# Kernel tuning notes

Measured on AMD Instinct MI355X. Metric: run time of the kernel, lower is better.

## Reference

```python
import jax, jax.numpy as jnp
import numpy as np

N, E = 50000, 1600000
IN, HID, HEADS, OUT = 128, 32, 4, 32
NEG_SLOPE = 0.2  # PyG GATConv default leaky_relu slope


def _glorot(k, shape):
    fan = shape[0] + shape[-1]
    return jax.random.normal(k, shape, dtype=jnp.float32) * np.sqrt(2.0 / fan).astype(np.float32)


def setup_inputs() -> dict:
    key = jax.random.key(0)
    ks = jax.random.split(key, 16)
    x = jax.random.normal(ks[0], (N, IN), dtype=jnp.float32)
    edge_index = jax.random.randint(ks[1], (2, E), 0, N, dtype=jnp.int32)
    # layer 0: in -> heads*hid, concat
    W0 = _glorot(ks[2], (IN, HEADS * HID))
    as0 = _glorot(ks[3], (HEADS, HID)); ad0 = _glorot(ks[4], (HEADS, HID))
    b0 = jnp.zeros((HEADS * HID,), jnp.float32)
    # layer 1: heads*hid -> heads*hid, concat
    W1 = _glorot(ks[5], (HEADS * HID, HEADS * HID))
    as1 = _glorot(ks[6], (HEADS, HID)); ad1 = _glorot(ks[7], (HEADS, HID))
    b1 = jnp.zeros((HEADS * HID,), jnp.float32)
    # layer 2: heads*hid -> out, heads=1, concat=False
    W2 = _glorot(ks[8], (HEADS * HID, OUT))
    as2 = _glorot(ks[9], (1, OUT)); ad2 = _glorot(ks[10], (1, OUT))
    b2 = jnp.zeros((OUT,), jnp.float32)
    return dict(x=x, edge_index=edge_index, W0=W0, as0=as0, ad0=ad0, b0=b0,
                W1=W1, as1=as1, ad1=ad1, b1=b1, W2=W2, as2=as2, ad2=ad2, b2=b2)


def gat_layer(x, src, dst, W, a_src, a_dst, b, heads, out_ch, concat):
    # linear transform per head: [N, heads, out_ch]
    h = (x @ W).reshape(N, heads, out_ch)
    # per-node attention half-logits: [N, heads]
    alpha_src = jnp.einsum('nhc,hc->nh', h, a_src)
    alpha_dst = jnp.einsum('nhc,hc->nh', h, a_dst)
    # per-edge logits (edge j -> i): [E', heads]
    logits = jax.nn.leaky_relu(alpha_src[src] + alpha_dst[dst], NEG_SLOPE)
    # segment softmax over incoming edges of each destination node
    m = jax.ops.segment_max(logits, dst, num_segments=N)
    e = jnp.exp(logits - m[dst])
    denom = jax.ops.segment_sum(e, dst, num_segments=N)
    alpha = e / denom[dst]
    # weighted message scatter-add: [N, heads, out_ch]
    out = jax.ops.segment_sum(h[src] * alpha[:, :, None], dst, num_segments=N)
    out = out.reshape(N, heads * out_ch) if concat else out.mean(axis=1)
    return out + b, alpha


def reference(x, edge_index, W0, as0, ad0, b0, W1, as1, ad1, b1, W2, as2, ad2, b2):
    # add self loops (PyG add_self_loops=True)
    loops = jnp.arange(N, dtype=edge_index.dtype)
    src = jnp.concatenate([edge_index[0], loops])
    dst = jnp.concatenate([edge_index[1], loops])

    h, alpha0 = gat_layer(x, src, dst, W0, as0, ad0, b0, HEADS, HID, True)
    h = jax.nn.elu(h)  # dropout inactive in eval mode
    h, _ = gat_layer(h, src, dst, W1, as1, ad1, b1, HEADS, HID, True)
    h = jax.nn.elu(h)
    out, _ = gat_layer(h, src, dst, W2, as2, ad2, b2, 1, OUT, False)
    return alpha0, out
```

## Files before the change

kernel.cpp:

```cpp
#include <hip/hip_runtime.h>
#include <math.h>

#define NN 50000
#define NEG 0.2f
#define TILE 4096

typedef __attribute__((ext_vector_type(8))) short short8;
typedef __attribute__((ext_vector_type(4))) float f32x4;

__device__ __forceinline__ unsigned short f2bf(float f){
    unsigned u = __float_as_uint(f);
    u += 0x7fffu + ((u >> 16) & 1u);
    return (unsigned short)(u >> 16);
}
__device__ __forceinline__ float bf2f(unsigned short v){
    return __uint_as_float(((unsigned)v) << 16);
}

__device__ __forceinline__ int excl_scan_256(int v, int* buf, int tid){
    buf[tid] = v;
    __syncthreads();
#pragma unroll
    for (int off = 1; off < 256; off <<= 1){
        int t = (tid >= off) ? buf[tid - off] : 0;
        __syncthreads();
        buf[tid] += t;
        __syncthreads();
    }
    return buf[tid] - v;
}

__global__ __launch_bounds__(256) void k_binning(const int* __restrict__ ei, int E,
        int* __restrict__ bucketCount, unsigned* __restrict__ tmp){
    __shared__ unsigned stage[TILE];
    __shared__ int hist[256], sbuf[256], exs[256], cur[256], gbase[256];
    int tid = threadIdx.x;
    int EP = E + NN;
    int tileBase = blockIdx.x * TILE;
    int cnt = min(TILE, EP - tileBase);

    hist[tid] = 0;
    __syncthreads();

    unsigned packed[16];
#pragma unroll
    for (int k = 0; k < 16; ++k){
        int e = tileBase + tid + (k << 8);
        unsigned p = 0xffffffffu;
        if (e < EP){
            int s, d;
            if (e < E){ s = ei[e]; d = ei[E + e]; } else { s = e - E; d = s; }
            p = ((unsigned)d << 16) | (unsigned)s;
            atomicAdd(&hist[d >> 8], 1);
        }
        packed[k] = p;
    }
    __syncthreads();
    int h = hist[tid];
    int ex = excl_scan_256(h, sbuf, tid);
    exs[tid] = ex;
    cur[tid] = ex;
    __syncthreads();
#pragma unroll
    for (int k = 0; k < 16; ++k){
        unsigned p = packed[k];
        if (p != 0xffffffffu){
            int b = p >> 24;
            int pos = atomicAdd(&cur[b], 1);
            stage[pos] = p;
        }
    }
    gbase[tid] = atomicAdd(&bucketCount[tid], h);
    __syncthreads();
    for (int i = tid; i < cnt; i += 256){
        unsigned p = stage[i];
        int b = p >> 24;
        tmp[(b << 14) + gbase[b] + (i - exs[b])] = p;
    }
}

__global__ __launch_bounds__(256) void k_bucket_csr(int EP,
        const int* __restrict__ bucketCount, const unsigned* __restrict__ tmp,
        int* __restrict__ row_ptr, unsigned short* __restrict__ ssrc){
    __shared__ int sbuf[256], deg[256], cur[256];
    __shared__ int baseSh, nSh;
    int b = blockIdx.x;
    int tid = threadIdx.x;
    int c = bucketCount[tid];
    int exb = excl_scan_256(c, sbuf, tid);
    if (tid == b){ baseSh = exb; nSh = c; }
    deg[tid] = 0;
    __syncthreads();
    int base = baseSh, n = nSh;
    const unsigned* tb = tmp + ((size_t)b << 14);
    for (int i = tid; i < n; i += 256)
        atomicAdd(&deg[(tb[i] >> 16) & 255], 1);
    __syncthreads();
    int d = deg[tid];
    int dx = excl_scan_256(d, sbuf, tid);
    cur[tid] = dx;
    int dst = (b << 8) + tid;
    if (dst < NN) row_ptr[dst] = base + dx;
    if (b == 0 && tid == 0) row_ptr[NN] = EP;
    __syncthreads();
    for (int i = tid; i < n; i += 256){
        unsigned p = tb[i];
        int pos = atomicAdd(&cur[(p >> 16) & 255], 1);
        ssrc[base + pos] = (unsigned short)(p & 0xffffu);
    }
}

__global__ void k_packW(const float* __restrict__ W0, const float* __restrict__ W1,
                        const float* __restrict__ W2,
                        unsigned short* __restrict__ h0, unsigned short* __restrict__ l0,
                        unsigned short* __restrict__ h1, unsigned short* __restrict__ l1,
                        unsigned short* __restrict__ h2, unsigned short* __restrict__ l2){
    int t = blockIdx.x * 256 + threadIdx.x;
    const float* W; unsigned short *ph, *pl; int Ncol; int u;
    if (t < 16384){ W = W0; ph = h0; pl = l0; Ncol = 128; u = t; }
    else if (t < 32768){ W = W1; ph = h1; pl = l1; Ncol = 128; u = t - 16384; }
    else if (t < 36864){ W = W2; ph = h2; pl = l2; Ncol = 32;  u = t - 32768; }
    else return;
    int n = u >> 7, k = u & 127;
    float f = W[k * Ncol + n];
    unsigned short hi = f2bf(f);
    unsigned short lo = f2bf(f - bf2f(hi));
    ph[n * 128 + k] = hi;
    pl[n * 128 + k] = lo;
}

template<int NT, int HH>
__global__ __launch_bounds__(256) void k_gemm_mfma(
        const float* __restrict__ A,
        const unsigned short* __restrict__ Bhi,
        const unsigned short* __restrict__ Blo,
        float* __restrict__ C, unsigned short* __restrict__ Cbf,
        const float* __restrict__ a_s,
        const float* __restrict__ a_d,
        float* __restrict__ asrc, float* __restrict__ adst,
        float* __restrict__ asrc_i, float* __restrict__ adst_i, int M){
    const int Ncol = NT * 16;
    int wave = threadIdx.x >> 6;
    int lane = threadIdx.x & 63;
    int r    = lane & 15;
    int oct  = lane >> 4;
    int rowBase = blockIdx.x * 64 + wave * 16;

    f32x4 acc[NT];
#pragma unroll
    for (int c = 0; c < NT; ++c) acc[c] = (f32x4){0.f, 0.f, 0.f, 0.f};

    int lrow = rowBase + r; if (lrow > M - 1) lrow = M - 1;
    const float* arow = A + (size_t)lrow * 128;

    for (int t = 0; t < 4; ++t){
        int k0 = t * 32 + oct * 8;
        float4 a0 = *(const float4*)&arow[k0];
        float4 a1 = *(const float4*)&arow[k0 + 4];
        float av[8] = {a0.x, a0.y, a0.z, a0.w, a1.x, a1.y, a1.z, a1.w};
        short8 ahi, alo;
#pragma unroll
        for (int j = 0; j < 8; ++j){
            unsigned short h = f2bf(av[j]);
            unsigned short l = f2bf(av[j] - bf2f(h));
            ahi[j] = (short)h; alo[j] = (short)l;
        }
#pragma unroll
        for (int c = 0; c < NT; ++c){
            short8 bhi = *(const short8*)&Bhi[(c * 16 + r) * 128 + k0];
            short8 blo = *(const short8*)&Blo[(c * 16 + r) * 128 + k0];
            acc[c] = __builtin_amdgcn_mfma_f32_16x16x32_bf16(ahi, bhi, acc[c], 0, 0, 0);
            acc[c] = __builtin_amdgcn_mfma_f32_16x16x32_bf16(alo, bhi, acc[c], 0, 0, 0);
            acc[c] = __builtin_amdgcn_mfma_f32_16x16x32_bf16(ahi, blo, acc[c], 0, 0, 0);
        }
    }
#pragma unroll
    for (int c = 0; c < NT; ++c){
#pragma unroll
        for (int reg = 0; reg < 4; ++reg){
            int row = rowBase + oct * 4 + reg;
            if (row < M){
                int colg = c * 16 + r;
                float v = acc[c][reg];
                if (C)   C[(size_t)row * Ncol + colg] = v;
                if (Cbf) Cbf[(size_t)(colg >> 5) * ((size_t)M * 32)
                             + (size_t)row * 32 + (colg & 31)] = f2bf(v);
            }
        }
    }

    float as_v[NT], ad_v[NT];
#pragma unroll
    for (int c = 0; c < NT; ++c){
        as_v[c] = a_s[c * 16 + r];
        ad_v[c] = a_d[c * 16 + r];
    }
    float vs[HH * 4], vd[HH * 4];
#pragma unroll
    for (int h = 0; h < HH; ++h)
#pragma unroll
        for (int reg = 0; reg < 4; ++reg){
            vs[h * 4 + reg] = acc[2 * h][reg] * as_v[2 * h]
                            + acc[2 * h + 1][reg] * as_v[2 * h + 1];
            vd[h * 4 + reg] = acc[2 * h][reg] * ad_v[2 * h]
                            + acc[2 * h + 1][reg] * ad_v[2 * h + 1];
        }
#pragma unroll
    for (int off = 1; off < 16; off <<= 1){
#pragma unroll
        for (int k = 0; k < HH * 4; ++k){
            vs[k] += __shfl_xor(vs[k], off);
            vd[k] += __shfl_xor(vd[k], off);
        }
    }
    if (HH == 4){
        int reg = r & 3, hd = r >> 2;
        int row = rowBase + oct * 4 + reg;
        if (row < M){
            asrc[hd * M + row] = vs[hd * 4 + reg];
            adst[hd * M + row] = vd[hd * 4 + reg];
            if (asrc_i){
                asrc_i[row * 4 + hd] = vs[hd * 4 + reg];
                adst_i[row * 4 + hd] = vd[hd * 4 + reg];
            }
        }
    } else {
        int reg = r & 3;
        int row = rowBase + oct * 4 + reg;
        if (row < M){
            if (r < 4)       asrc[row] = vs[reg];
            else if (r < 8)  adst[row] = vd[reg];
        }
    }
}

__global__ __launch_bounds__(256) void k_aggh4(
        const uint4* __restrict__ hb4,
        const float* __restrict__ asrc,
        const float* __restrict__ adst,
        const int* __restrict__ row_ptr, const unsigned short* __restrict__ ssrc,
        const float* __restrict__ bias, float* __restrict__ outp,
        float* __restrict__ gdenom, int writeStats){
    int b  = blockIdx.x;
    int h  = (b >> 1) & 3;
    int kh = (b >> 3) * 2 + (b & 1);
    int wave = threadIdx.x >> 6;
    int lane = threadIdx.x & 63;
    int ns = lane >> 4;
    int g  = (lane >> 2) & 3;
    int q  = lane & 3;
    int i  = kh * 16 + wave * 4 + ns;
    bool valid = (i < NN);
    int iv = valid ? i : NN - 1;
    int lo = row_ptr[iv], hi = row_ptr[iv + 1];
    float adv = adst[h * NN + iv];
    const uint4* hp = hb4 + (size_t)h * ((size_t)NN * 4);
    const float* ap = asrc + h * NN;

    float acc[8];
#pragma unroll
    for (int k = 0; k < 8; ++k) acc[k] = 0.f;
    float dsum = 0.f;

#define AGH_FMA(AA, GV) {                                                     \
        acc[0] += (AA) * __uint_as_float((GV).x << 16);                       \
        acc[1] += (AA) * __uint_as_float((GV).x & 0xffff0000u);               \
        acc[2] += (AA) * __uint_as_float((GV).y << 16);                       \
        acc[3] += (AA) * __uint_as_float((GV).y & 0xffff0000u);               \
        acc[4] += (AA) * __uint_as_float((GV).z << 16);                       \
        acc[5] += (AA) * __uint_as_float((GV).z & 0xffff0000u);               \
        acc[6] += (AA) * __uint_as_float((GV).w << 16);                       \
        acc[7] += (AA) * __uint_as_float((GV).w & 0xffff0000u); }
#define AGH_ONE(JJ) {                                                         \
        float lg_ = ap[(JJ)] + adv;                                           \
        lg_ = fmaxf(lg_, NEG * lg_);                                          \
        float a_ = __expf(lg_);                                               \
        dsum += a_;                                                           \
        uint4 gv_ = hp[(JJ) * 4u + (unsigned)q];                              \
        AGH_FMA(a_, gv_) }

    int idx = lo;
    if (lo & 1){
        if (g == 0){ unsigned j = ssrc[lo]; AGH_ONE(j) }
        idx = lo + 1;
    }
    for (; idx + 16 <= hi; idx += 16){
        unsigned pA = *(const unsigned*)&ssrc[idx + 2 * g];
        unsigned pB = *(const unsigned*)&ssrc[idx + 8 + 2 * g];
        unsigned j0 = pA & 0xffffu, j1 = pA >> 16;
        unsigned j2 = pB & 0xffffu, j3 = pB >> 16;
        float s0 = ap[j0], s1 = ap[j1], s2 = ap[j2], s3 = ap[j3];
        uint4 v0 = hp[j0 * 4u + (unsigned)q];
        uint4 v1 = hp[j1 * 4u + (unsigned)q];
        uint4 v2 = hp[j2 * 4u + (unsigned)q];
        uint4 v3 = hp[j3 * 4u + (unsigned)q];
        float lg0 = s0 + adv; lg0 = fmaxf(lg0, NEG * lg0);
        float lg1 = s1 + adv; lg1 = fmaxf(lg1, NEG * lg1);
        float lg2 = s2 + adv; lg2 = fmaxf(lg2, NEG * lg2);
        float lg3 = s3 + adv; lg3 = fmaxf(lg3, NEG * lg3);
        float a0 = __expf(lg0), a1 = __expf(lg1);
        float a2 = __expf(lg2), a3 = __expf(lg3);
        dsum += (a0 + a1) + (a2 + a3);
        AGH_FMA(a0, v0)
        AGH_FMA(a1, v1)
        AGH_FMA(a2, v2)
        AGH_FMA(a3, v3)
    }
    if (idx + 8 <= hi){
        unsigned pA = *(const unsigned*)&ssrc[idx + 2 * g];
        unsigned j0 = pA & 0xffffu, j1 = pA >> 16;
        float s0 = ap[j0], s1 = ap[j1];
        uint4 v0 = hp[j0 * 4u + (unsigned)q];
        uint4 v1 = hp[j1 * 4u + (unsigned)q];
        float lg0 = s0 + adv; lg0 = fmaxf(lg0, NEG * lg0);
        float lg1 = s1 + adv; lg1 = fmaxf(lg1, NEG * lg1);
        float a0 = __expf(lg0), a1 = __expf(lg1);
        dsum += a0 + a1;
        AGH_FMA(a0, v0)
        AGH_FMA(a1, v1)
        idx += 8;
    }
    {
        int k0 = idx + 2 * g, k1 = k0 + 1;
        if (k0 < hi){ unsigned j = ssrc[k0]; AGH_ONE(j) }
        if (k1 < hi){ unsigned j = ssrc[k1]; AGH_ONE(j) }
    }
#undef AGH_ONE
#undef AGH_FMA
#pragma unroll
    for (int k = 0; k < 8; ++k){
        acc[k] += __shfl_xor(acc[k], 4);
        acc[k] += __shfl_xor(acc[k], 8);
    }
    dsum += __shfl_xor(dsum, 4);
    dsum += __shfl_xor(dsum, 8);

    if (writeStats && g == 0 && q == 0 && valid)
        gdenom[i * 4 + h] = dsum;

    if (g == 0 && valid){
        float rs = 1.f / dsum;
        int c0 = h * 32 + q * 8;
        float4 bA = *(const float4*)&bias[c0];
        float4 bB = *(const float4*)&bias[c0 + 4];
        float o[8] = {acc[0] * rs + bA.x, acc[1] * rs + bA.y,
                      acc[2] * rs + bA.z, acc[3] * rs + bA.w,
                      acc[4] * rs + bB.x, acc[5] * rs + bB.y,
                      acc[6] * rs + bB.z, acc[7] * rs + bB.w};
#pragma unroll
        for (int k = 0; k < 8; ++k)
            o[k] = (o[k] > 0.f) ? o[k] : (__expf(o[k]) - 1.f);
        *(float4*)&outp[(size_t)i * 128 + c0]     = make_float4(o[0], o[1], o[2], o[3]);
        *(float4*)&outp[(size_t)i * 128 + c0 + 4] = make_float4(o[4], o[5], o[6], o[7]);
    }
}

__global__ void k_alpha0(const int* __restrict__ ei, int E,
                         const float4* __restrict__ asrc4, const float4* __restrict__ adst4,
                         const float4* __restrict__ gd4, float4* __restrict__ out){
    int e = blockIdx.x * 256 + threadIdx.x;
    int EP = E + NN;
    if (e >= EP) return;
    int s, d;
    if (e < E){ s = ei[e]; d = ei[E + e]; } else { s = e - E; d = s; }
    float4 as = asrc4[s], ad = adst4[d], dn = gd4[d];
    float4 r;
    float lg;
    lg = as.x + ad.x; lg = fmaxf(lg, NEG * lg); r.x = __expf(lg) / dn.x;
    lg = as.y + ad.y; lg = fmaxf(lg, NEG * lg); r.y = __expf(lg) / dn.y;
    lg = as.z + ad.z; lg = fmaxf(lg, NEG * lg); r.z = __expf(lg) / dn.z;
    lg = as.w + ad.w; lg = fmaxf(lg, NEG * lg); r.w = __expf(lg) / dn.w;
    out[e] = r;
}

__global__ __launch_bounds__(256) void k_agg1b(
        const uint4* __restrict__ hb,
        const float* __restrict__ asrc, const float* __restrict__ adst,
        const int* __restrict__ row_ptr, const unsigned short* __restrict__ ssrc,
        const float* __restrict__ bias, float* __restrict__ outp){
    int wave = threadIdx.x >> 6;
    int lane = threadIdx.x & 63;
    int ns = lane >> 4;
    int g  = (lane >> 2) & 3;
    int q  = lane & 3;
    int i  = blockIdx.x * 16 + wave * 4 + ns;
    bool valid = (i < NN);
    int iv = valid ? i : NN - 1;
    int lo = row_ptr[iv], hi = row_ptr[iv + 1];
    float adv = adst[iv];

    float acc[8];
#pragma unroll
    for (int k = 0; k < 8; ++k) acc[k] = 0.f;
    float dsum = 0.f;

#define AGB_FMA(AA, GV) {                                                     \
        acc[0] += (AA) * __uint_as_float((GV).x << 16);                       \
        acc[1] += (AA) * __uint_as_float((GV).x & 0xffff0000u);               \
        acc[2] += (AA) * __uint_as_float((GV).y << 16);                       \
        acc[3] += (AA) * __uint_as_float((GV).y & 0xffff0000u);               \
        acc[4] += (AA) * __uint_as_float((GV).z << 16);                       \
        acc[5] += (AA) * __uint_as_float((GV).z & 0xffff0000u);               \
        acc[6] += (AA) * __uint_as_float((GV).w << 16);                       \
        acc[7] += (AA) * __uint_as_float((GV).w & 0xffff0000u); }
#define AGB_ONE(JJ) {                                                         \
        float lg_ = asrc[(JJ)] + adv;                                         \
        lg_ = fmaxf(lg_, NEG * lg_);                                          \
        float a_ = __expf(lg_);                                               \
        dsum += a_;                                                           \
        uint4 gv_ = hb[(JJ) * 4u + (unsigned)q];                              \
        AGB_FMA(a_, gv_) }

    int idx = lo;
    if (lo & 1){
        if (g == 0){ unsigned j = ssrc[lo]; AGB_ONE(j) }
        idx = lo + 1;
    }
    for (; idx + 16 <= hi; idx += 16){
        unsigned pA = *(const unsigned*)&ssrc[idx + 2 * g];
        unsigned pB = *(const unsigned*)&ssrc[idx + 8 + 2 * g];
        unsigned j0 = pA & 0xffffu, j1 = pA >> 16;
        unsigned j2 = pB & 0xffffu, j3 = pB >> 16;
        float s0 = asrc[j0], s1 = asrc[j1], s2 = asrc[j2], s3 = asrc[j3];
        uint4 v0 = hb[j0 * 4u + (unsigned)q];
        uint4 v1 = hb[j1 * 4u + (unsigned)q];
        uint4 v2 = hb[j2 * 4u + (unsigned)q];
        uint4 v3 = hb[j3 * 4u + (unsigned)q];
        float lg0 = s0 + adv; lg0 = fmaxf(lg0, NEG * lg0);
        float lg1 = s1 + adv; lg1 = fmaxf(lg1, NEG * lg1);
        float lg2 = s2 + adv; lg2 = fmaxf(lg2, NEG * lg2);
        float lg3 = s3 + adv; lg3 = fmaxf(lg3, NEG * lg3);
        float a0 = __expf(lg0), a1 = __expf(lg1);
        float a2 = __expf(lg2), a3 = __expf(lg3);
        dsum += (a0 + a1) + (a2 + a3);
        AGB_FMA(a0, v0)
        AGB_FMA(a1, v1)
        AGB_FMA(a2, v2)
        AGB_FMA(a3, v3)
    }
    if (idx + 8 <= hi){
        unsigned pA = *(const unsigned*)&ssrc[idx + 2 * g];
        unsigned j0 = pA & 0xffffu, j1 = pA >> 16;
        float s0 = asrc[j0], s1 = asrc[j1];
        uint4 v0 = hb[j0 * 4u + (unsigned)q];
        uint4 v1 = hb[j1 * 4u + (unsigned)q];
        float lg0 = s0 + adv; lg0 = fmaxf(lg0, NEG * lg0);
        float lg1 = s1 + adv; lg1 = fmaxf(lg1, NEG * lg1);
        float a0 = __expf(lg0), a1 = __expf(lg1);
        dsum += a0 + a1;
        AGB_FMA(a0, v0)
        AGB_FMA(a1, v1)
        idx += 8;
    }
    {
        int k0 = idx + 2 * g, k1 = k0 + 1;
        if (k0 < hi){ unsigned j = ssrc[k0]; AGB_ONE(j) }
        if (k1 < hi){ unsigned j = ssrc[k1]; AGB_ONE(j) }
    }
#undef AGB_ONE
#undef AGB_FMA
#pragma unroll
    for (int k = 0; k < 8; ++k){
        acc[k] += __shfl_xor(acc[k], 4);
        acc[k] += __shfl_xor(acc[k], 8);
    }
    dsum += __shfl_xor(dsum, 4);
    dsum += __shfl_xor(dsum, 8);

    if (g == 0 && valid){
        float rs = 1.f / dsum;
        int c0 = q * 8;
        float4 bA = *(const float4*)&bias[c0];
        float4 bB = *(const float4*)&bias[c0 + 4];
        *(float4*)&outp[(size_t)i * 32 + c0] =
            make_float4(acc[0] * rs + bA.x, acc[1] * rs + bA.y,
                        acc[2] * rs + bA.z, acc[3] * rs + bA.w);
        *(float4*)&outp[(size_t)i * 32 + c0 + 4] =
            make_float4(acc[4] * rs + bB.x, acc[5] * rs + bB.y,
                        acc[6] * rs + bB.z, acc[7] * rs + bB.w);
    }
}

extern "C" void kernel_launch(void* const* d_in, const int* in_sizes, int n_in,
                              void* d_out, int out_size, void* d_ws, size_t ws_size,
                              hipStream_t stream){
    const float* x   = (const float*)d_in[0];
    const int*   ei  = (const int*)  d_in[1];
    const float* W0  = (const float*)d_in[2];
    const float* as0 = (const float*)d_in[3];
    const float* ad0 = (const float*)d_in[4];
    const float* b0  = (const float*)d_in[5];
    const float* W1  = (const float*)d_in[6];
    const float* as1 = (const float*)d_in[7];
    const float* ad1 = (const float*)d_in[8];
    const float* b1  = (const float*)d_in[9];
    const float* W2  = (const float*)d_in[10];
    const float* as2 = (const float*)d_in[11];
    const float* ad2 = (const float*)d_in[12];
    const float* b2  = (const float*)d_in[13];

    const int E  = in_sizes[1] / 2;
    const int EP = E + NN;

    char* w = (char*)d_ws;
    size_t off = 0;
    auto carve = [&](size_t bytes) -> char* {
        char* p = w + off;
        off += (bytes + 255) & ~(size_t)255;
        return p;
    };
    int*            bucketCount = (int*)       carve(sizeof(int) * 256);
    int*            row_ptr = (int*)           carve(sizeof(int) * (NN + 1));
    unsigned short* ssrc    = (unsigned short*)carve(sizeof(short) * ((size_t)EP + 2));
    unsigned short* hb2     = (unsigned short*)carve(sizeof(short) * (size_t)NN * 32);
    unsigned short* hb16    = (unsigned short*)carve(sizeof(short) * (size_t)NN * 128);
    float*          post    = (float*)         carve(sizeof(float) * (size_t)NN * 128);
    float*          asrc    = (float*)         carve(sizeof(float) * NN * 4);
    float*          adst    = (float*)         carve(sizeof(float) * NN * 4);
    float*          asrci   = (float*)         carve(sizeof(float) * NN * 4);
    float*          adsti   = (float*)         carve(sizeof(float) * NN * 4);
    float*          gdenom  = (float*)         carve(sizeof(float) * NN * 4);
    unsigned short* Whi0    = (unsigned short*)carve(sizeof(short) * 16384);
    unsigned short* Wlo0    = (unsigned short*)carve(sizeof(short) * 16384);
    unsigned short* Whi1    = (unsigned short*)carve(sizeof(short) * 16384);
    unsigned short* Wlo1    = (unsigned short*)carve(sizeof(short) * 16384);
    unsigned short* Whi2    = (unsigned short*)carve(sizeof(short) * 4096);
    unsigned short* Wlo2    = (unsigned short*)carve(sizeof(short) * 4096);
    unsigned*       tmp     = (unsigned*)post;

    float* out_alpha = (float*)d_out;
    float* out_final = (float*)d_out + (size_t)EP * 4;

    const int edgeBlocks = (EP + 255) / 256;
    const int aggBlocks  = 12504;
    const int agg1Blocks = (NN + 15) / 16;
    const int gemmBlocks = (NN + 63) / 64;

    hipMemsetAsync(bucketCount, 0, sizeof(int) * 256, stream);
    k_binning   <<<(EP + TILE - 1) / TILE, 256, 0, stream>>>(ei, E, bucketCount, tmp);
    k_bucket_csr<<<256, 256, 0, stream>>>(EP, bucketCount, tmp, row_ptr, ssrc);
    k_packW     <<<144, 256, 0, stream>>>(W0, W1, W2, Whi0, Wlo0, Whi1, Wlo1, Whi2, Wlo2);

    k_gemm_mfma<8, 4><<<gemmBlocks, 256, 0, stream>>>(x, Whi0, Wlo0,
        nullptr, hb16, as0, ad0, asrc, adst, asrci, adsti, NN);
    k_aggh4<<<aggBlocks, 256, 0, stream>>>((const uint4*)hb16, asrc, adst, row_ptr,
                                           ssrc, b0, post, gdenom, 1);
    k_alpha0<<<edgeBlocks, 256, 0, stream>>>(ei, E, (const float4*)asrci,
                                             (const float4*)adsti,
                                             (const float4*)gdenom, (float4*)out_alpha);

    k_gemm_mfma<8, 4><<<gemmBlocks, 256, 0, stream>>>(post, Whi1, Wlo1,
        nullptr, hb16, as1, ad1, asrc, adst, nullptr, nullptr, NN);
    k_aggh4<<<aggBlocks, 256, 0, stream>>>((const uint4*)hb16, asrc, adst, row_ptr,
                                           ssrc, b1, post, gdenom, 0);

    k_gemm_mfma<2, 1><<<gemmBlocks, 256, 0, stream>>>(post, Whi2, Wlo2,
        nullptr, hb2, as2, ad2, asrc, adst, nullptr, nullptr, NN);
    k_agg1b<<<agg1Blocks, 256, 0, stream>>>((const uint4*)hb2, asrc, adst, row_ptr,
                                            ssrc, b2, out_final);
}
```

Measured before the change: 411.6 us.

## Sort destination nodes by in-degree to balance aggregation waves

Adds a degree histogram, scan and scatter pass that builds a permutation of destination nodes sorted by descending in-degree. The aggregation kernels then process nodes through this permutation, so nodes handled by the same wave have similar edge counts and lanes sit idle less. The cost is three small extra kernel launches and an extra memset, plus loss of locality in the row_ptr/adst/output accesses, since consecutive lanes now touch scattered node indices. With random-graph degrees (mean around 33, Poisson-like) the variance is modest, so the gain from better balance is limited.

```diff
diff --git a/kernel.cpp b/kernel.cpp
--- a/kernel.cpp
+++ b/kernel.cpp
@@ -108,6 +108,31 @@
         int pos = atomicAdd(&cur[(p >> 16) & 255], 1);
         ssrc[base + pos] = (unsigned short)(p & 0xffffu);
     }
+}
+
+__global__ __launch_bounds__(256) void k_deghist(const int* __restrict__ row_ptr,
+                                                 int* __restrict__ hist){
+    int i = blockIdx.x * 256 + threadIdx.x;
+    if (i >= NN) return;
+    int d = row_ptr[i + 1] - row_ptr[i];
+    atomicAdd(&hist[min(d, 255)], 1);
+}
+__global__ __launch_bounds__(256) void k_degscan(const int* __restrict__ hist,
+                                                 int* __restrict__ cur){
+    __shared__ int sbuf[256];
+    int tid = threadIdx.x;
+    int v = hist[255 - tid];
+    int ex = excl_scan_256(v, sbuf, tid);
+    cur[255 - tid] = ex;
+}
+__global__ __launch_bounds__(256) void k_degscatter(const int* __restrict__ row_ptr,
+                                                    int* __restrict__ cur,
+                                                    int* __restrict__ perm){
+    int i = blockIdx.x * 256 + threadIdx.x;
+    if (i >= NN) return;
+    int d = row_ptr[i + 1] - row_ptr[i];
+    int pos = atomicAdd(&cur[min(d, 255)], 1);
+    perm[pos] = i;
 }
 
 __global__ void k_packW(const float* __restrict__ W0, const float* __restrict__ W1,
@@ -239,6 +264,7 @@
         const float* __restrict__ asrc,
         const float* __restrict__ adst,
         const int* __restrict__ row_ptr, const unsigned short* __restrict__ ssrc,
+        const int* __restrict__ perm,
         const float* __restrict__ bias, float* __restrict__ outp,
         float* __restrict__ gdenom, int writeStats){
     int b  = blockIdx.x;
@@ -249,11 +275,11 @@
     int ns = lane >> 4;
     int g  = (lane >> 2) & 3;
     int q  = lane & 3;
-    int i  = kh * 16 + wave * 4 + ns;
-    bool valid = (i < NN);
-    int iv = valid ? i : NN - 1;
-    int lo = row_ptr[iv], hi = row_ptr[iv + 1];
-    float adv = adst[h * NN + iv];
+    int k_ = kh * 16 + wave * 4 + ns;
+    bool valid = (k_ < NN);
+    int i = perm[valid ? k_ : NN - 1];
+    int lo = row_ptr[i], hi = row_ptr[i + 1];
+    float adv = adst[h * NN + i];
     const uint4* hp = hb4 + (size_t)h * ((size_t)NN * 4);
     const float* ap = asrc + h * NN;
 
@@ -377,17 +403,18 @@
         const uint4* __restrict__ hb,
         const float* __restrict__ asrc, const float* __restrict__ adst,
         const int* __restrict__ row_ptr, const unsigned short* __restrict__ ssrc,
+        const int* __restrict__ perm,
         const float* __restrict__ bias, float* __restrict__ outp){
     int wave = threadIdx.x >> 6;
     int lane = threadIdx.x & 63;
     int ns = lane >> 4;
     int g  = (lane >> 2) & 3;
     int q  = lane & 3;
-    int i  = blockIdx.x * 16 + wave * 4 + ns;
-    bool valid = (i < NN);
-    int iv = valid ? i : NN - 1;
-    int lo = row_ptr[iv], hi = row_ptr[iv + 1];
-    float adv = adst[iv];
+    int k_ = blockIdx.x * 16 + wave * 4 + ns;
+    bool valid = (k_ < NN);
+    int i = perm[valid ? k_ : NN - 1];
+    int lo = row_ptr[i], hi = row_ptr[i + 1];
+    float adv = adst[i];
 
     float acc[8];
 #pragma unroll
@@ -520,6 +547,9 @@
     float*          asrci   = (float*)         carve(sizeof(float) * NN * 4);
     float*          adsti   = (float*)         carve(sizeof(float) * NN * 4);
     float*          gdenom  = (float*)         carve(sizeof(float) * NN * 4);
+    int*            perm    = (int*)           carve(sizeof(int) * NN);
+    int*            dhist   = (int*)           carve(sizeof(int) * 256);
+    int*            dcur    = (int*)           carve(sizeof(int) * 256);
     unsigned short* Whi0    = (unsigned short*)carve(sizeof(short) * 16384);
     unsigned short* Wlo0    = (unsigned short*)carve(sizeof(short) * 16384);
     unsigned short* Whi1    = (unsigned short*)carve(sizeof(short) * 16384);
@@ -532,19 +562,24 @@
     float* out_final = (float*)d_out + (size_t)EP * 4;
 
     const int edgeBlocks = (EP + 255) / 256;
+    const int nodeBlocks = (NN + 255) / 256;
     const int aggBlocks  = 12504;
     const int agg1Blocks = (NN + 15) / 16;
     const int gemmBlocks = (NN + 63) / 64;
 
     hipMemsetAsync(bucketCount, 0, sizeof(int) * 256, stream);
+    hipMemsetAsync(dhist, 0, sizeof(int) * 256, stream);
     k_binning   <<<(EP + TILE - 1) / TILE, 256, 0, stream>>>(ei, E, bucketCount, tmp);
     k_bucket_csr<<<256, 256, 0, stream>>>(EP, bucketCount, tmp, row_ptr, ssrc);
+    k_deghist   <<<nodeBlocks, 256, 0, stream>>>(row_ptr, dhist);
+    k_degscan   <<<1, 256, 0, stream>>>(dhist, dcur);
+    k_degscatter<<<nodeBlocks, 256, 0, stream>>>(row_ptr, dcur, perm);
     k_packW     <<<144, 256, 0, stream>>>(W0, W1, W2, Whi0, Wlo0, Whi1, Wlo1, Whi2, Wlo2);
 
     k_gemm_mfma<8, 4><<<gemmBlocks, 256, 0, stream>>>(x, Whi0, Wlo0,
         nullptr, hb16, as0, ad0, asrc, adst, asrci, adsti, NN);
     k_aggh4<<<aggBlocks, 256, 0, stream>>>((const uint4*)hb16, asrc, adst, row_ptr,
-                                           ssrc, b0, post, gdenom, 1);
+                                           ssrc, perm, b0, post, gdenom, 1);
     k_alpha0<<<edgeBlocks, 256, 0, stream>>>(ei, E, (const float4*)asrci,
                                              (const float4*)adsti,
                                              (const float4*)gdenom, (float4*)out_alpha);
@@ -552,10 +587,10 @@
     k_gemm_mfma<8, 4><<<gemmBlocks, 256, 0, stream>>>(post, Whi1, Wlo1,
         nullptr, hb16, as1, ad1, asrc, adst, nullptr, nullptr, NN);
     k_aggh4<<<aggBlocks, 256, 0, stream>>>((const uint4*)hb16, asrc, adst, row_ptr,
-                                           ssrc, b1, post, gdenom, 0);
+                                           ssrc, perm, b1, post, gdenom, 0);
 
     k_gemm_mfma<2, 1><<<gemmBlocks, 256, 0, stream>>>(post, Whi2, Wlo2,
         nullptr, hb2, as2, ad2, asrc, adst, nullptr, nullptr, NN);
     k_agg1b<<<agg1Blocks, 256, 0, stream>>>((const uint4*)hb2, asrc, adst, row_ptr,
-                                            ssrc, b2, out_final);
-}
+                                            ssrc, perm, b2, out_final);
+}
```

New measurement: 633.8 us. 1.54x slower.
